# Kernel optimization log

Measured on AMD Instinct MI355X. Metric: run time of the kernel, lower is better.

Reference implementation:

```python
import jax, jax.numpy as jnp
import numpy as np

MIN_EXPERTS = 1
MAX_EXPERTS = 8
TEMPERATURE = 1.0


def setup_inputs() -> dict:
    key = jax.random.key(0)
    ks = jax.random.split(key, 7)
    B, S, H, E = 8, 4096, 1024, 64
    Hh = H // 2
    return {
        "hidden_states": jax.random.normal(ks[0], (B, S, H), dtype=jnp.float32),
        "W_router": jax.random.normal(ks[1], (E, H), dtype=jnp.float32) * 0.02,
        "b_router": jax.random.normal(ks[2], (E,), dtype=jnp.float32) * 0.02,
        "W1": jax.random.normal(ks[3], (Hh, H), dtype=jnp.float32) * 0.02,
        "b1": jax.random.normal(ks[4], (Hh,), dtype=jnp.float32) * 0.02,
        "W2": jax.random.normal(ks[5], (1, Hh), dtype=jnp.float32) * 0.02,
        "b2": jax.random.normal(ks[6], (1,), dtype=jnp.float32) * 0.02,
    }


def reference(hidden_states, W_router, b_router, W1, b1, W2, b2):
    B, S, H = hidden_states.shape
    flat = hidden_states.reshape(-1, H)                     # [N, H]

    # router logits
    router_logits = (flat @ W_router.T + b_router) / TEMPERATURE  # [N, E]

    # confidence net: Linear -> ReLU -> Linear -> Sigmoid
    h = jax.nn.relu(flat @ W1.T + b1)                       # [N, H/2]
    confidence = jax.nn.sigmoid(h @ W2.T + b2).squeeze(-1)  # [N]

    # dynamic k per token (torch.round = half-to-even, same as jnp.round)
    dk = MIN_EXPERTS + (MAX_EXPERTS - MIN_EXPERTS) * (1.0 - confidence)
    dk = jnp.clip(jnp.round(dk), MIN_EXPERTS, MAX_EXPERTS).astype(jnp.int32)  # [N]

    routing_probs = jax.nn.softmax(router_logits, axis=-1)  # [N, E]

    # single top-k pass replaces per-iteration sort; mask slots >= dynamic_k
    top_vals, top_idx = jax.lax.top_k(routing_probs, MAX_EXPERTS)  # [N, max_k]
    slot = jnp.arange(MAX_EXPERTS, dtype=jnp.int32)[None, :]       # [1, max_k]
    active = slot < dk[:, None]                                    # [N, max_k]
    sel_w = jnp.where(active, top_vals, 0.0)
    sel_i = jnp.where(active, top_idx, 0).astype(jnp.int64)

    sel_w = sel_w.reshape(B, S, MAX_EXPERTS)
    sel_i = sel_i.reshape(B, S, MAX_EXPERTS)
    return sel_w, sel_i, confidence, router_logits
```

## Files before the change

### kernel.cpp

```cpp
#include <hip/hip_runtime.h>
#include <hip/hip_bf16.h>
#include <math.h>

#define N_TOK 32768
#define HDIM 1024
#define HH 512
#define NOUT 576
#define BM 128
#define BN 64
#define BK 32
#define THREADS 256
#define KC 384

#define OFF_SELW 0
#define OFF_SELI 262144
#define OFF_CONF 524288
#define OFF_LOG  557056

__device__ float  g_Bmat[HDIM * NOUT];
__device__ double g_partial[N_TOK * 8];

__global__ __launch_bounds__(256) void k_build(const float* __restrict__ W1,
                                               const float* __restrict__ Wr) {
  int idx = blockIdx.x * 256 + threadIdx.x;
  int k = idx / NOUT;
  int j = idx - k * NOUT;
  float v = (j < HH) ? W1[(size_t)j * HDIM + k] : Wr[(size_t)(j - HH) * HDIM + k];
  g_Bmat[idx] = v;
}

__global__ __launch_bounds__(THREADS) void k_gemm(const float* __restrict__ A,
                                                  const float* __restrict__ b1,
                                                  const float* __restrict__ W2,
                                                  const float* __restrict__ b_router,
                                                  float* __restrict__ out_logits) {
  __shared__ float As[BK][BM];
  __shared__ float Bs[BK][BN];

  int bid = blockIdx.x;
  int xcd = bid & 7;
  int s   = bid >> 3;
  int j   = s % 9;
  int t   = xcd + 8 * (s / 9);

  const int tid = threadIdx.x;
  const int tx  = tid & 15;
  const int ty  = tid >> 4;
  const int m0  = t * BM;
  const int n0  = j * BN;

  float acc[8][4];
  float carry[8][4];
  #pragma unroll
  for (int i = 0; i < 8; ++i)
    #pragma unroll
    for (int c = 0; c < 4; ++c) { acc[i][c] = 0.f; carry[i][c] = 0.f; }

  const int arow = tid >> 1;
  const int akc  = tid & 1;
  const float* Ag = A + (size_t)(m0 + arow) * HDIM + akc * 16;

  for (int k0 = 0; k0 < HDIM; k0 += BK) {
    if (k0 == KC || k0 == 2 * KC) {
      #pragma unroll
      for (int i = 0; i < 8; ++i)
        #pragma unroll
        for (int c = 0; c < 4; ++c) {
          carry[i][c] = carry[i][c] + acc[i][c];
          acc[i][c] = 0.f;
        }
    }

    float4 av[4];
    #pragma unroll
    for (int c = 0; c < 4; ++c)
      av[c] = *(const float4*)(Ag + k0 + c * 4);
    float4 bv[2];
    #pragma unroll
    for (int c = 0; c < 2; ++c) {
      int idx = tid + c * 256;
      int kr  = idx >> 4;
      int ch  = idx & 15;
      bv[c] = *(const float4*)&g_Bmat[(size_t)(k0 + kr) * NOUT + n0 + ch * 4];
    }
    __syncthreads();
    #pragma unroll
    for (int c = 0; c < 4; ++c) {
      int kb = akc * 16 + c * 4;
      As[kb + 0][arow] = av[c].x;
      As[kb + 1][arow] = av[c].y;
      As[kb + 2][arow] = av[c].z;
      As[kb + 3][arow] = av[c].w;
    }
    #pragma unroll
    for (int c = 0; c < 2; ++c) {
      int idx = tid + c * 256;
      int kr  = idx >> 4;
      int ch  = idx & 15;
      *(float4*)&Bs[kr][ch * 4] = bv[c];
    }
    __syncthreads();

    #pragma unroll 4
    for (int kk = 0; kk < BK; ++kk) {
      float4 a03 = *(const float4*)&As[kk][ty * 8 + 0];
      float4 a47 = *(const float4*)&As[kk][ty * 8 + 4];
      float a[8] = {a03.x, a03.y, a03.z, a03.w, a47.x, a47.y, a47.z, a47.w};
      float b[4];
      b[0] = Bs[kk][tx * 4 + 0];
      b[1] = Bs[kk][tx * 4 + 1];
      b[2] = Bs[kk][tx * 4 + 2];
      b[3] = Bs[kk][tx * 4 + 3];
      #pragma unroll
      for (int i = 0; i < 8; ++i)
        #pragma unroll
        for (int c = 0; c < 4; ++c)
          acc[i][c] = fmaf(a[i], b[c], acc[i][c]);
    }
  }

  float res[8][4];
  #pragma unroll
  for (int i = 0; i < 8; ++i)
    #pragma unroll
    for (int c = 0; c < 4; ++c) res[i][c] = carry[i][c] + acc[i][c];

  if (j < 8) {
    double w2v[4];
    float  b1v[4];
    #pragma unroll
    for (int c = 0; c < 4; ++c) {
      w2v[c] = (double)W2[n0 + tx * 4 + c];
      b1v[c] = b1[n0 + tx * 4 + c];
    }
    #pragma unroll
    for (int i = 0; i < 8; ++i) {
      double sacc = 0.0;
      #pragma unroll
      for (int c = 0; c < 4; ++c) {
        float h = fmaxf(res[i][c] + b1v[c], 0.f);
        sacc = fma((double)h, w2v[c], sacc);
      }
      sacc += __shfl_xor(sacc, 1, 64);
      sacc += __shfl_xor(sacc, 2, 64);
      sacc += __shfl_xor(sacc, 4, 64);
      sacc += __shfl_xor(sacc, 8, 64);
      if (tx == 0) g_partial[(size_t)(m0 + ty * 8 + i) * 8 + j] = sacc;
    }
  } else {
    float brv[4];
    #pragma unroll
    for (int c = 0; c < 4; ++c) brv[c] = b_router[tx * 4 + c];
    #pragma unroll
    for (int i = 0; i < 8; ++i) {
      int row = m0 + ty * 8 + i;
      float o[4];
      #pragma unroll
      for (int c = 0; c < 4; ++c) o[c] = res[i][c] + brv[c];
      *(float4*)&out_logits[(size_t)row * 64 + tx * 4] =
          make_float4(o[0], o[1], o[2], o[3]);
    }
  }
}

__global__ __launch_bounds__(256) void k_post(const float* __restrict__ b2,
                                              float* __restrict__ d_out) {
  const int lane = threadIdx.x & 63;
  const int wave = threadIdx.x >> 6;
  const int q    = lane & 7;
  const int tsub = lane >> 3;
  const int tk   = blockIdx.x * 32 + wave * 8 + tsub;

  double p = g_partial[(size_t)tk * 8 + q];
  p += __shfl_xor(p, 1, 64);
  p += __shfl_xor(p, 2, 64);
  p += __shfl_xor(p, 4, 64);
  double ca   = (double)b2[0] + p;
  double conf = 1.0 / (1.0 + exp(-ca));
  double dkf  = 1.0 + 7.0 * (1.0 - conf);
  double dkr  = rint(dkf);
  int dk = (int)fmin(fmax(dkr, 1.0), 8.0);

  const float* logits = d_out + OFF_LOG + (size_t)tk * 64;
  float l[8];
  #pragma unroll
  for (int b = 0; b < 8; ++b) l[b] = logits[b * 8 + q];

  float mx = l[0];
  #pragma unroll
  for (int b = 1; b < 8; ++b) mx = fmaxf(mx, l[b]);
  mx = fmaxf(mx, __shfl_xor(mx, 1, 64));
  mx = fmaxf(mx, __shfl_xor(mx, 2, 64));
  mx = fmaxf(mx, __shfl_xor(mx, 4, 64));

  float ex[8];
  #pragma unroll
  for (int b = 0; b < 8; ++b) ex[b] = expf(l[b] - mx);

  float r = ex[0];
  #pragma unroll
  for (int b = 1; b < 8; ++b) r += ex[b];
  r += __shfl_xor(r, 1, 64);
  r += __shfl_xor(r, 2, 64);
  float ssum = r + __shfl_xor(r, 4, 64);

  float v[8];
  #pragma unroll
  for (int b = 0; b < 8; ++b) v[b] = ex[b] / ssum;

  float myw = 0.f, myi = 0.f;
  unsigned used = 0u;
  #pragma unroll
  for (int slot = 0; slot < 8; ++slot) {
    float best = -1.f;
    int   bi   = 64;
    #pragma unroll
    for (int b = 0; b < 8; ++b) {
      bool ok = (((used >> b) & 1u) == 0u) && (v[b] > best);
      best = ok ? v[b] : best;
      bi   = ok ? (b * 8 + q) : bi;
    }
    #pragma unroll
    for (int m = 1; m <= 4; m <<= 1) {
      float ow = __shfl_xor(best, m, 64);
      int   oi = __shfl_xor(bi,   m, 64);
      bool take = (ow > best) || (ow == best && oi < bi);
      best = take ? ow : best;
      bi   = take ? oi : bi;
    }
    if ((bi & 7) == q) used |= (1u << (bi >> 3));
    bool active = slot < dk;
    if (slot == q) {
      myw = active ? best : 0.f;
      myi = active ? (float)bi : 0.f;
    }
  }

  d_out[OFF_SELW + (size_t)tk * 8 + q] = myw;
  d_out[OFF_SELI + (size_t)tk * 8 + q] = myi;
  if (q == 0) d_out[OFF_CONF + tk] = (float)conf;
}

extern "C" void kernel_launch(void* const* d_in, const int* in_sizes, int n_in,
                              void* d_out, int out_size, void* d_ws, size_t ws_size,
                              hipStream_t stream) {
  const float* hidden   = (const float*)d_in[0];
  const float* W_router = (const float*)d_in[1];
  const float* b_router = (const float*)d_in[2];
  const float* W1       = (const float*)d_in[3];
  const float* b1       = (const float*)d_in[4];
  const float* W2       = (const float*)d_in[5];
  const float* b2       = (const float*)d_in[6];
  float* out = (float*)d_out;

  k_build<<<(HDIM * NOUT) / 256, 256, 0, stream>>>(W1, W_router);
  k_gemm<<<(N_TOK / BM) * 9, THREADS, 0, stream>>>(hidden, b1, W2, b_router,
                                                   out + OFF_LOG);
  k_post<<<N_TOK / 256 / 128 * 128 ? (N_TOK / 32) : (N_TOK / 32), 256, 0, stream>>>(b2, out);
}
```

Measured before the change: 680.9 us.

## Enlarge GEMM tile to 256x64 with 8x8 per-thread output and double-buffered LDS

Doubles the M tile so each thread computes an 8x8 block, using vectorized B reads from shared memory. Adds ping-pong LDS buffers with register prefetch of the next K slice, cutting one barrier per iteration. The aim is higher FMA-to-load ratio and overlap of global loads with compute. The cost is higher register pressure and fewer blocks, which may worsen occupancy and tail balance.

```diff
diff --git a/kernel.cpp b/kernel.cpp
--- a/kernel.cpp
+++ b/kernel.cpp
@@ -6,7 +6,7 @@
 #define HDIM 1024
 #define HH 512
 #define NOUT 576
-#define BM 128
+#define BM 256
 #define BN 64
 #define BK 32
 #define THREADS 256
@@ -29,13 +29,13 @@
   g_Bmat[idx] = v;
 }
 
-__global__ __launch_bounds__(THREADS) void k_gemm(const float* __restrict__ A,
-                                                  const float* __restrict__ b1,
-                                                  const float* __restrict__ W2,
-                                                  const float* __restrict__ b_router,
-                                                  float* __restrict__ out_logits) {
-  __shared__ float As[BK][BM];
-  __shared__ float Bs[BK][BN];
+__global__ __launch_bounds__(THREADS, 2) void k_gemm(const float* __restrict__ A,
+                                                     const float* __restrict__ b1,
+                                                     const float* __restrict__ W2,
+                                                     const float* __restrict__ b_router,
+                                                     float* __restrict__ out_logits) {
+  __shared__ float As[2][BK][BM];
+  __shared__ float Bs[2][BK][BN];
 
   int bid = blockIdx.x;
   int xcd = bid & 7;
@@ -44,121 +44,151 @@
   int t   = xcd + 8 * (s / 9);
 
   const int tid = threadIdx.x;
-  const int tx  = tid & 15;
-  const int ty  = tid >> 4;
+  const int tx  = tid & 7;
+  const int ty  = tid >> 3;
   const int m0  = t * BM;
   const int n0  = j * BN;
 
-  float acc[8][4];
-  float carry[8][4];
+  float acc[8][8];
+  float carry[8][8];
   #pragma unroll
   for (int i = 0; i < 8; ++i)
     #pragma unroll
-    for (int c = 0; c < 4; ++c) { acc[i][c] = 0.f; carry[i][c] = 0.f; }
-
-  const int arow = tid >> 1;
-  const int akc  = tid & 1;
-  const float* Ag = A + (size_t)(m0 + arow) * HDIM + akc * 16;
-
+    for (int c = 0; c < 8; ++c) { acc[i][c] = 0.f; carry[i][c] = 0.f; }
+
+  const float* Ag = A + (size_t)(m0 + tid) * HDIM;
+
+  float4 av[8];
+  float4 bv[2];
+
+  #pragma unroll
+  for (int c = 0; c < 8; ++c) av[c] = *(const float4*)(Ag + c * 4);
+  #pragma unroll
+  for (int c = 0; c < 2; ++c) {
+    int g  = tid + c * 256;
+    int kr = g >> 4;
+    int ch = g & 15;
+    bv[c] = *(const float4*)&g_Bmat[(size_t)kr * NOUT + n0 + ch * 4];
+  }
+  #pragma unroll
+  for (int c = 0; c < 8; ++c) {
+    int kb = c * 4;
+    As[0][kb + 0][tid] = av[c].x;
+    As[0][kb + 1][tid] = av[c].y;
+    As[0][kb + 2][tid] = av[c].z;
+    As[0][kb + 3][tid] = av[c].w;
+  }
+  #pragma unroll
+  for (int c = 0; c < 2; ++c) {
+    int g  = tid + c * 256;
+    int kr = g >> 4;
+    int ch = g & 15;
+    *(float4*)&Bs[0][kr][ch * 4] = bv[c];
+  }
+  __syncthreads();
+
+  int p = 0;
   for (int k0 = 0; k0 < HDIM; k0 += BK) {
+    const bool not_last = (k0 + BK < HDIM);
+
+    if (not_last) {
+      #pragma unroll
+      for (int c = 0; c < 8; ++c) av[c] = *(const float4*)(Ag + (k0 + BK) + c * 4);
+      #pragma unroll
+      for (int c = 0; c < 2; ++c) {
+        int g  = tid + c * 256;
+        int kr = g >> 4;
+        int ch = g & 15;
+        bv[c] = *(const float4*)&g_Bmat[(size_t)(k0 + BK + kr) * NOUT + n0 + ch * 4];
+      }
+    }
+
     if (k0 == KC || k0 == 2 * KC) {
       #pragma unroll
       for (int i = 0; i < 8; ++i)
         #pragma unroll
-        for (int c = 0; c < 4; ++c) {
+        for (int c = 0; c < 8; ++c) {
           carry[i][c] = carry[i][c] + acc[i][c];
           acc[i][c] = 0.f;
         }
     }
 
-    float4 av[4];
-    #pragma unroll
-    for (int c = 0; c < 4; ++c)
-      av[c] = *(const float4*)(Ag + k0 + c * 4);
-    float4 bv[2];
-    #pragma unroll
-    for (int c = 0; c < 2; ++c) {
-      int idx = tid + c * 256;
-      int kr  = idx >> 4;
-      int ch  = idx & 15;
-      bv[c] = *(const float4*)&g_Bmat[(size_t)(k0 + kr) * NOUT + n0 + ch * 4];
-    }
-    __syncthreads();
-    #pragma unroll
-    for (int c = 0; c < 4; ++c) {
-      int kb = akc * 16 + c * 4;
-      As[kb + 0][arow] = av[c].x;
-      As[kb + 1][arow] = av[c].y;
-      As[kb + 2][arow] = av[c].z;
-      As[kb + 3][arow] = av[c].w;
-    }
-    #pragma unroll
-    for (int c = 0; c < 2; ++c) {
-      int idx = tid + c * 256;
-      int kr  = idx >> 4;
-      int ch  = idx & 15;
-      *(float4*)&Bs[kr][ch * 4] = bv[c];
-    }
-    __syncthreads();
-
-    #pragma unroll 4
+    #pragma unroll 2
     for (int kk = 0; kk < BK; ++kk) {
-      float4 a03 = *(const float4*)&As[kk][ty * 8 + 0];
-      float4 a47 = *(const float4*)&As[kk][ty * 8 + 4];
+      float4 a03 = *(const float4*)&As[p][kk][ty * 8 + 0];
+      float4 a47 = *(const float4*)&As[p][kk][ty * 8 + 4];
+      float4 b03 = *(const float4*)&Bs[p][kk][tx * 8 + 0];
+      float4 b47 = *(const float4*)&Bs[p][kk][tx * 8 + 4];
       float a[8] = {a03.x, a03.y, a03.z, a03.w, a47.x, a47.y, a47.z, a47.w};
-      float b[4];
-      b[0] = Bs[kk][tx * 4 + 0];
-      b[1] = Bs[kk][tx * 4 + 1];
-      b[2] = Bs[kk][tx * 4 + 2];
-      b[3] = Bs[kk][tx * 4 + 3];
+      float b[8] = {b03.x, b03.y, b03.z, b03.w, b47.x, b47.y, b47.z, b47.w};
       #pragma unroll
       for (int i = 0; i < 8; ++i)
         #pragma unroll
-        for (int c = 0; c < 4; ++c)
+        for (int c = 0; c < 8; ++c)
           acc[i][c] = fmaf(a[i], b[c], acc[i][c]);
     }
-  }
-
-  float res[8][4];
+
+    if (not_last) {
+      #pragma unroll
+      for (int c = 0; c < 8; ++c) {
+        int kb = c * 4;
+        As[p ^ 1][kb + 0][tid] = av[c].x;
+        As[p ^ 1][kb + 1][tid] = av[c].y;
+        As[p ^ 1][kb + 2][tid] = av[c].z;
+        As[p ^ 1][kb + 3][tid] = av[c].w;
+      }
+      #pragma unroll
+      for (int c = 0; c < 2; ++c) {
+        int g  = tid + c * 256;
+        int kr = g >> 4;
+        int ch = g & 15;
+        *(float4*)&Bs[p ^ 1][kr][ch * 4] = bv[c];
+      }
+      __syncthreads();
+      p ^= 1;
+    }
+  }
+
   #pragma unroll
   for (int i = 0; i < 8; ++i)
     #pragma unroll
-    for (int c = 0; c < 4; ++c) res[i][c] = carry[i][c] + acc[i][c];
+    for (int c = 0; c < 8; ++c) carry[i][c] = carry[i][c] + acc[i][c];
 
   if (j < 8) {
-    double w2v[4];
-    float  b1v[4];
-    #pragma unroll
-    for (int c = 0; c < 4; ++c) {
-      w2v[c] = (double)W2[n0 + tx * 4 + c];
-      b1v[c] = b1[n0 + tx * 4 + c];
+    double w2v[8];
+    float  b1v[8];
+    #pragma unroll
+    for (int c = 0; c < 8; ++c) {
+      w2v[c] = (double)W2[n0 + tx * 8 + c];
+      b1v[c] = b1[n0 + tx * 8 + c];
     }
     #pragma unroll
     for (int i = 0; i < 8; ++i) {
       double sacc = 0.0;
       #pragma unroll
-      for (int c = 0; c < 4; ++c) {
-        float h = fmaxf(res[i][c] + b1v[c], 0.f);
+      for (int c = 0; c < 8; ++c) {
+        float h = fmaxf(carry[i][c] + b1v[c], 0.f);
         sacc = fma((double)h, w2v[c], sacc);
       }
       sacc += __shfl_xor(sacc, 1, 64);
       sacc += __shfl_xor(sacc, 2, 64);
       sacc += __shfl_xor(sacc, 4, 64);
-      sacc += __shfl_xor(sacc, 8, 64);
       if (tx == 0) g_partial[(size_t)(m0 + ty * 8 + i) * 8 + j] = sacc;
     }
   } else {
-    float brv[4];
-    #pragma unroll
-    for (int c = 0; c < 4; ++c) brv[c] = b_router[tx * 4 + c];
+    float brv[8];
+    #pragma unroll
+    for (int c = 0; c < 8; ++c) brv[c] = b_router[tx * 8 + c];
     #pragma unroll
     for (int i = 0; i < 8; ++i) {
       int row = m0 + ty * 8 + i;
-      float o[4];
-      #pragma unroll
-      for (int c = 0; c < 4; ++c) o[c] = res[i][c] + brv[c];
-      *(float4*)&out_logits[(size_t)row * 64 + tx * 4] =
+      float o[8];
+      #pragma unroll
+      for (int c = 0; c < 8; ++c) o[c] = carry[i][c] + brv[c];
+      *(float4*)&out_logits[(size_t)row * 64 + tx * 8 + 0] =
           make_float4(o[0], o[1], o[2], o[3]);
+      *(float4*)&out_logits[(size_t)row * 64 + tx * 8 + 4] =
+          make_float4(o[4], o[5], o[6], o[7]);
     }
   }
 }
@@ -256,5 +286,5 @@
   k_build<<<(HDIM * NOUT) / 256, 256, 0, stream>>>(W1, W_router);
   k_gemm<<<(N_TOK / BM) * 9, THREADS, 0, stream>>>(hidden, b1, W2, b_router,
                                                    out + OFF_LOG);
-  k_post<<<N_TOK / 256 / 128 * 128 ? (N_TOK / 32) : (N_TOK / 32), 256, 0, stream>>>(b2, out);
-}
+  k_post<<<N_TOK / 32, 256, 0, stream>>>(b2, out);
+}
```

New measurement: 727.1 us. 6.8% more time.
